# Optimization experiments

Hardware: AMD Instinct MI355X
Metric: run time of the kernel (lower is better)

## Reference

```python
import jax, jax.numpy as jnp
import numpy as np

NUM_EXPERTS = 8
TOP_K = 2


def setup_inputs() -> dict:
    key = jax.random.key(0)
    ks = jax.random.split(key, 5)
    B, S, H, F, E = 2, 2048, 1024, 4096, NUM_EXPERTS
    return {
        "hidden_states": jax.random.normal(ks[0], (B, S, H), dtype=jnp.float32),
        "router_w": jax.random.normal(ks[1], (H, E), dtype=jnp.float32) * 0.02,
        "router_b": jnp.zeros((E,), dtype=jnp.float32),
        "w1": jax.random.normal(ks[2], (E, H, F), dtype=jnp.float32) * 0.02,
        "b1": jnp.zeros((E, F), dtype=jnp.float32),
        "w2": jax.random.normal(ks[3], (E, F, H), dtype=jnp.float32) * 0.02,
        "b2": jnp.zeros((E, H), dtype=jnp.float32),
    }


def reference(hidden_states, router_w, router_b, w1, b1, w2, b2):
    # Router: softmax over experts, take top-2, renormalize.
    logits = jnp.einsum("bsh,he->bse", hidden_states, router_w) + router_b
    probs = jax.nn.softmax(logits, axis=-1)
    top_w, top_i = jax.lax.top_k(probs, TOP_K)              # [B,S,2]
    top_w = top_w / jnp.sum(top_w, axis=-1, keepdims=True)
    # Combine weights per expert: [B,S,E] (sum of slot weights where routed).
    combine = jnp.sum(
        top_w[..., None] * jax.nn.one_hot(top_i, NUM_EXPERTS, dtype=top_w.dtype),
        axis=-2,
    )
    # Dense expert FFN over stacked experts (grouped GEMM form).
    h = jax.nn.gelu(
        jnp.einsum("bsh,ehf->ebsf", hidden_states, w1) + b1[:, None, None, :],
        approximate=False,
    )  # exact GELU matches torch nn.GELU default
    y = jnp.einsum("ebsf,efh->ebsh", h, w2) + b2[:, None, None, :]
    # Weighted combine of top-2 expert outputs per token.
    return jnp.einsum("bse,ebsh->bsh", combine, y)
```

## Files before the change

kernel.cpp:

```cpp
#include <hip/hip_runtime.h>
#include <hip/hip_bf16.h>
#include <stdint.h>

#define T_TOKENS 4096
#define H_DIM    1024
#define F_DIM    4096
#define NE       8
#define NA       8192

typedef __bf16 bf16x8 __attribute__((ext_vector_type(8)));
typedef float  f32x4  __attribute__((ext_vector_type(4)));

__device__ __forceinline__ float b2f(unsigned short u) {
    union { float f; uint32_t i; } v; v.i = ((uint32_t)u) << 16; return v.f;
}
__device__ __forceinline__ unsigned short f2b(float f) {
    union { float f; uint32_t i; } v; v.f = f;
    uint32_t x = v.i;
    return (unsigned short)((x + 0x7FFFu + ((x >> 16) & 1u)) >> 16);
}

__global__ void probe_kernel(const unsigned short* __restrict__ hs,
                             int* __restrict__ flag) {
    int lane = threadIdx.x;
    int cnt = 0;
    for (int j = 0; j < 16; j++) {
        unsigned short u = hs[(lane * 16 + j) * 2];
        int e = (u >> 7) & 0xFF;
        if (e >= 100 && e <= 135) cnt++;
    }
    for (int off = 32; off > 0; off >>= 1) cnt += __shfl_down(cnt, off);
    if (lane == 0) *flag = (cnt >= 512) ? 0 : 1;
}

__global__ __launch_bounds__(256) void conv_hs_kernel(
    const void* __restrict__ hs, const int* __restrict__ flag,
    unsigned short* __restrict__ out) {
    size_t idx = ((size_t)blockIdx.x * 256 + threadIdx.x) * 8;
    if (*flag) {
        const float* p = (const float*)hs + idx;
        float4 a = *(const float4*)p, b = *(const float4*)(p + 4);
        ushort4 o0, o1;
        o0.x = f2b(a.x); o0.y = f2b(a.y); o0.z = f2b(a.z); o0.w = f2b(a.w);
        o1.x = f2b(b.x); o1.y = f2b(b.y); o1.z = f2b(b.z); o1.w = f2b(b.w);
        *(ushort4*)(out + idx) = o0;
        *(ushort4*)(out + idx + 4) = o1;
    } else {
        *(uint4*)(out + idx) = *(const uint4*)((const unsigned short*)hs + idx);
    }
}

__global__ __launch_bounds__(256) void router_kernel(
    const void* __restrict__ hs, const void* __restrict__ rw,
    const void* __restrict__ rb, const int* __restrict__ flag,
    int* __restrict__ top_i, float* __restrict__ top_w) {
    bool f32 = (*flag != 0);
    int wave = threadIdx.x >> 6, lane = threadIdx.x & 63;
    int t = blockIdx.x * 4 + wave;
    float acc[NE];
#pragma unroll
    for (int e = 0; e < NE; e++) acc[e] = 0.f;
    if (f32) {
        const float* hrow = (const float*)hs + (size_t)t * H_DIM;
        const float* rwf = (const float*)rw;
        for (int j = 0; j < 16; j++) {
            int k = j * 64 + lane;
            float h = hrow[k];
            float4 a = *(const float4*)(rwf + (size_t)k * NE);
            float4 b = *(const float4*)(rwf + (size_t)k * NE + 4);
            acc[0] += h * a.x; acc[1] += h * a.y; acc[2] += h * a.z; acc[3] += h * a.w;
            acc[4] += h * b.x; acc[5] += h * b.y; acc[6] += h * b.z; acc[7] += h * b.w;
        }
    } else {
        const unsigned short* hrow = (const unsigned short*)hs + (size_t)t * H_DIM;
        const unsigned short* rwu = (const unsigned short*)rw;
        for (int j = 0; j < 16; j++) {
            int k = j * 64 + lane;
            float h = b2f(hrow[k]);
            uint4 rv = *(const uint4*)(rwu + (size_t)k * NE);
            const unsigned short* rs = (const unsigned short*)&rv;
#pragma unroll
            for (int e = 0; e < NE; e++) acc[e] += h * b2f(rs[e]);
        }
    }
#pragma unroll
    for (int e = 0; e < NE; e++)
        for (int off = 32; off > 0; off >>= 1) acc[e] += __shfl_down(acc[e], off);
    if (lane == 0) {
        float lg[NE];
#pragma unroll
        for (int e = 0; e < NE; e++)
            lg[e] = acc[e] + (f32 ? ((const float*)rb)[e]
                                  : b2f(((const unsigned short*)rb)[e]));
        int e0 = 0;
        for (int e = 1; e < NE; e++) if (lg[e] > lg[e0]) e0 = e;
        int e1 = (e0 == 0) ? 1 : 0;
        for (int e = 0; e < NE; e++) if (e != e0 && lg[e] > lg[e1]) e1 = e;
        float w0 = 1.f / (1.f + expf(lg[e1] - lg[e0]));
        top_i[t * 2] = e0; top_i[t * 2 + 1] = e1;
        top_w[t * 2] = w0; top_w[t * 2 + 1] = 1.f - w0;
    }
}

__global__ __launch_bounds__(256) void assign_kernel(
    const int* __restrict__ top_i, const float* __restrict__ top_w,
    int* __restrict__ token_list, float* __restrict__ wgt_list,
    int* __restrict__ assign_row, int* __restrict__ counts,
    int* __restrict__ offsets) {
    __shared__ int cnt_s[NE], cur_s[NE];
    int tid = threadIdx.x;
    if (tid < NE) cnt_s[tid] = 0;
    __syncthreads();
    for (int idx = tid; idx < NA; idx += 256) atomicAdd(&cnt_s[top_i[idx]], 1);
    __syncthreads();
    if (tid == 0) {
        int run = 0;
        for (int e = 0; e < NE; e++) {
            offsets[e] = run; counts[e] = cnt_s[e]; cur_s[e] = run; run += cnt_s[e];
        }
    }
    __syncthreads();
    for (int idx = tid; idx < NA; idx += 256) {
        int e = top_i[idx];
        int pos = atomicAdd(&cur_s[e], 1);
        token_list[pos] = idx >> 1;
        wgt_list[pos] = top_w[idx];
        assign_row[idx] = pos;
    }
}

__global__ __launch_bounds__(256) void transpose_kernel(
    const void* __restrict__ in, unsigned short* __restrict__ out,
    int R, int C, const int* __restrict__ flag) {
    bool f32 = (*flag != 0);
    size_t zo = (size_t)blockIdx.z * R * C;
    int c0 = blockIdx.x * 64, r0 = blockIdx.y * 64;
    __shared__ unsigned short t[64][65];
    int tx = threadIdx.x & 31, ty = threadIdx.x >> 5;
    if (f32) {
        const float* inf = (const float*)in + zo;
#pragma unroll
        for (int i = 0; i < 8; i++) {
            int r = ty + i * 8;
            float2 v = *(const float2*)&inf[(size_t)(r0 + r) * C + c0 + tx * 2];
            t[r][tx * 2] = f2b(v.x); t[r][tx * 2 + 1] = f2b(v.y);
        }
    } else {
        const unsigned short* inu = (const unsigned short*)in + zo;
#pragma unroll
        for (int i = 0; i < 8; i++) {
            int r = ty + i * 8;
            ushort2 v = *(const ushort2*)&inu[(size_t)(r0 + r) * C + c0 + tx * 2];
            t[r][tx * 2] = v.x; t[r][tx * 2 + 1] = v.y;
        }
    }
    __syncthreads();
#pragma unroll
    for (int i = 0; i < 8; i++) {
        int cc = ty + i * 8;
        ushort2 w; w.x = t[tx * 2][cc]; w.y = t[tx * 2 + 1][cc];
        *(ushort2*)&out[zo + (size_t)(c0 + cc) * R + r0 + tx * 2] = w;
    }
}

template <int MODE>
__global__ __launch_bounds__(256) void gemm_kernel(
    const unsigned short* __restrict__ Abase,
    const unsigned short* __restrict__ Bt,
    const void* __restrict__ bias,
    const int* __restrict__ flag,
    const int* __restrict__ token_list, const float* __restrict__ wgt_list,
    const int* __restrict__ counts, const int* __restrict__ offsets,
    unsigned short* __restrict__ act_out, unsigned short* __restrict__ y_out) {
    constexpr int K    = (MODE == 0) ? H_DIM : F_DIM;
    constexpr int NDIM = (MODE == 0) ? F_DIM : H_DIM;
    constexpr int AST  = (MODE == 0) ? H_DIM : F_DIM;

    const int e = blockIdx.z;
    const int cnt = counts[e];
    const int m0 = blockIdx.y * 128;
    if (m0 >= cnt) return;
    const int off = offsets[e];
    const int n0 = blockIdx.x * 128;
    const bool f32 = (*flag != 0);

    __shared__ __bf16 As[128 * 64];
    __shared__ __bf16 Bs[128 * 64];
    __shared__ int   tok_s[128];
    __shared__ float wgt_s[128];

    const int tid = threadIdx.x;
    const int wave = tid >> 6, lane = tid & 63;

    if (tid < 128) {
        int r = off + min(m0 + tid, cnt - 1);
        tok_s[tid] = (MODE == 0) ? token_list[r] : r;
        wgt_s[tid] = wgt_list[r];
    }
    __syncthreads();

    const int c = tid & 7;
    const int rsub = tid >> 3;
    const unsigned short* Bexp = Bt + (size_t)e * NDIM * K;
    size_t gofsA[4], gofsB[4];
    uint32_t lofs[4];
#pragma unroll
    for (int i = 0; i < 4; i++) {
        int r = i * 32 + rsub;
        int arow = tok_s[r];
        gofsA[i] = (size_t)arow * AST + c * 8;
        gofsB[i] = (size_t)(n0 + r) * K + c * 8;
        lofs[i] = r * 64 + ((c ^ (r & 7)) * 8);
    }

    f32x4 acc[4][4];
#pragma unroll
    for (int i = 0; i < 4; i++)
#pragma unroll
        for (int j = 0; j < 4; j++) acc[i][j] = (f32x4){0.f, 0.f, 0.f, 0.f};

    const int wr = wave >> 1, wc = wave & 1;
    const int lane15 = lane & 15, quad = lane >> 4;

    for (int kt = 0; kt < K / 64; kt++) {
        bf16x8 va[4], vb[4];
#pragma unroll
        for (int i = 0; i < 4; i++)
            va[i] = *(const bf16x8*)(Abase + gofsA[i] + (size_t)kt * 64);
#pragma unroll
        for (int i = 0; i < 4; i++)
            vb[i] = *(const bf16x8*)(Bexp + gofsB[i] + (size_t)kt * 64);
        __syncthreads();
#pragma unroll
        for (int i = 0; i < 4; i++) *(bf16x8*)(As + lofs[i]) = va[i];
#pragma unroll
        for (int i = 0; i < 4; i++) *(bf16x8*)(Bs + lofs[i]) = vb[i];
        __syncthreads();
#pragma unroll
        for (int kk = 0; kk < 2; kk++) {
            bf16x8 a[4], b[4];
#pragma unroll
            for (int i = 0; i < 4; i++) {
                int row = wr * 64 + i * 16 + lane15;
                int koff = (kk * 32 + quad * 8) ^ ((row & 7) * 8);
                a[i] = *(const bf16x8*)&As[row * 64 + koff];
            }
#pragma unroll
            for (int j = 0; j < 4; j++) {
                int row = wc * 64 + j * 16 + lane15;
                int koff = (kk * 32 + quad * 8) ^ ((row & 7) * 8);
                b[j] = *(const bf16x8*)&Bs[row * 64 + koff];
            }
#pragma unroll
            for (int i = 0; i < 4; i++)
#pragma unroll
                for (int j = 0; j < 4; j++)
                    acc[i][j] = __builtin_amdgcn_mfma_f32_16x16x32_bf16(a[i], b[j], acc[i][j], 0, 0, 0);
        }
    }

#pragma unroll
    for (int j = 0; j < 4; j++) {
        int col = n0 + wc * 64 + j * 16 + lane15;
        float bv = f32 ? ((const float*)bias)[(size_t)e * NDIM + col]
                       : b2f(((const unsigned short*)bias)[(size_t)e * NDIM + col]);
#pragma unroll
        for (int i = 0; i < 4; i++) {
#pragma unroll
            for (int r = 0; r < 4; r++) {
                int rowl = wr * 64 + i * 16 + quad * 4 + r;
                if (m0 + rowl < cnt) {
                    float v = acc[i][j][r] + bv;
                    if (MODE == 0) {
                        v = 0.5f * v * (1.f + erff(v * 0.70710678118f));
                        act_out[(size_t)(off + m0 + rowl) * F_DIM + col] = f2b(v);
                    } else {
                        y_out[(size_t)(off + m0 + rowl) * H_DIM + col] = f2b(v * wgt_s[rowl]);
                    }
                }
            }
        }
    }
}

__global__ __launch_bounds__(256) void combine_kernel(
    const unsigned short* __restrict__ y, const int* __restrict__ assign_row,
    void* __restrict__ out, const int* __restrict__ flag) {
    bool f32 = (*flag != 0);
    int t = blockIdx.x;
    int r0 = assign_row[t * 2], r1 = assign_row[t * 2 + 1];
    ushort4 a = ((const ushort4*)(y + (size_t)r0 * H_DIM))[threadIdx.x];
    ushort4 b = ((const ushort4*)(y + (size_t)r1 * H_DIM))[threadIdx.x];
    float s0 = b2f(a.x) + b2f(b.x), s1 = b2f(a.y) + b2f(b.y);
    float s2 = b2f(a.z) + b2f(b.z), s3 = b2f(a.w) + b2f(b.w);
    if (f32) {
        float4 o = {s0, s1, s2, s3};
        ((float4*)out)[(size_t)t * (H_DIM / 4) + threadIdx.x] = o;
    } else {
        ushort4 o;
        o.x = f2b(s0); o.y = f2b(s1); o.z = f2b(s2); o.w = f2b(s3);
        ((ushort4*)((unsigned short*)out + (size_t)t * H_DIM))[threadIdx.x] = o;
    }
}

extern "C" void kernel_launch(void* const* d_in, const int* in_sizes, int n_in,
                              void* d_out, int out_size, void* d_ws, size_t ws_size,
                              hipStream_t stream) {
    const void* hs = d_in[0];
    const void* rw = d_in[1];
    const void* rb = d_in[2];
    const void* w1 = d_in[3];
    const void* b1 = d_in[4];
    const void* w2 = d_in[5];
    const void* b2 = d_in[6];

    char* ws = (char*)d_ws;
    size_t o = 0;
    auto alloc = [&](size_t bytes) {
        char* p = ws + o; o += (bytes + 255) & ~(size_t)255; return p;
    };
    unsigned short* wt   = (unsigned short*)alloc((size_t)NE * F_DIM * H_DIM * 2);
    unsigned short* act  = (unsigned short*)alloc((size_t)NA * F_DIM * 2);
    unsigned short* yb   = (unsigned short*)alloc((size_t)NA * H_DIM * 2);
    unsigned short* hsb  = (unsigned short*)alloc((size_t)T_TOKENS * H_DIM * 2);
    int*   top_i      = (int*)alloc(NA * 4);
    float* top_w      = (float*)alloc(NA * 4);
    int*   token_list = (int*)alloc(NA * 4);
    float* wgt_list   = (float*)alloc(NA * 4);
    int*   assign_row = (int*)alloc(NA * 4);
    int*   counts     = (int*)alloc(64);
    int*   offsets    = (int*)alloc(64);
    int*   flag       = (int*)alloc(64);
    (void)ws_size; (void)in_sizes; (void)n_in; (void)out_size;

    probe_kernel<<<1, 64, 0, stream>>>((const unsigned short*)hs, flag);
    conv_hs_kernel<<<T_TOKENS * H_DIM / 2048, 256, 0, stream>>>(hs, flag, hsb);
    router_kernel<<<T_TOKENS / 4, 256, 0, stream>>>(hs, rw, rb, flag, top_i, top_w);
    assign_kernel<<<1, 256, 0, stream>>>(top_i, top_w, token_list, wgt_list,
                                         assign_row, counts, offsets);
    transpose_kernel<<<dim3(F_DIM / 64, H_DIM / 64, NE), 256, 0, stream>>>(
        w1, wt, H_DIM, F_DIM, flag);
    gemm_kernel<0><<<dim3(F_DIM / 128, T_TOKENS / 128, NE), 256, 0, stream>>>(
        hsb, wt, b1, flag, token_list, wgt_list, counts, offsets, act, nullptr);
    transpose_kernel<<<dim3(H_DIM / 64, F_DIM / 64, NE), 256, 0, stream>>>(
        w2, wt, F_DIM, H_DIM, flag);
    gemm_kernel<1><<<dim3(H_DIM / 128, T_TOKENS / 128, NE), 256, 0, stream>>>(
        act, wt, b2, flag, token_list, wgt_list, counts, offsets, nullptr, yb);
    combine_kernel<<<T_TOKENS, 256, 0, stream>>>(yb, assign_row, d_out, flag);
}
```

Measured before the change: 702.4 us.

## Load GEMM tiles directly into LDS, fuse bf16 conversion into router, shrink FFN2 tile

The GEMM kernel now stages A and B tiles with global_load_lds, which writes straight into LDS and skips the register round trip. The swizzled chunk layout is kept so the existing MFMA fragment reads still match, and the trailing barrier moves to the end of each k-step. The separate hidden-state bf16 conversion kernel is removed; the router writes the bf16 copy while it reads the rows. The second GEMM uses a 64-row M tile with a larger grid to give it more blocks, at the cost of less reuse of B per block.

```diff
diff --git a/kernel.cpp b/kernel.cpp
--- a/kernel.cpp
+++ b/kernel.cpp
@@ -18,6 +18,13 @@
     union { float f; uint32_t i; } v; v.f = f;
     uint32_t x = v.i;
     return (unsigned short)((x + 0x7FFFu + ((x >> 16) & 1u)) >> 16);
+}
+
+__device__ __forceinline__ void gl_lds16(const void* g, void* l) {
+    __builtin_amdgcn_global_load_lds(
+        (const __attribute__((address_space(1))) void*)g,
+        (__attribute__((address_space(3))) void*)l,
+        16, 0, 0);
 }
 
 __global__ void probe_kernel(const unsigned short* __restrict__ hs,
@@ -33,30 +40,15 @@
     if (lane == 0) *flag = (cnt >= 512) ? 0 : 1;
 }
 
-__global__ __launch_bounds__(256) void conv_hs_kernel(
-    const void* __restrict__ hs, const int* __restrict__ flag,
-    unsigned short* __restrict__ out) {
-    size_t idx = ((size_t)blockIdx.x * 256 + threadIdx.x) * 8;
-    if (*flag) {
-        const float* p = (const float*)hs + idx;
-        float4 a = *(const float4*)p, b = *(const float4*)(p + 4);
-        ushort4 o0, o1;
-        o0.x = f2b(a.x); o0.y = f2b(a.y); o0.z = f2b(a.z); o0.w = f2b(a.w);
-        o1.x = f2b(b.x); o1.y = f2b(b.y); o1.z = f2b(b.z); o1.w = f2b(b.w);
-        *(ushort4*)(out + idx) = o0;
-        *(ushort4*)(out + idx + 4) = o1;
-    } else {
-        *(uint4*)(out + idx) = *(const uint4*)((const unsigned short*)hs + idx);
-    }
-}
-
 __global__ __launch_bounds__(256) void router_kernel(
     const void* __restrict__ hs, const void* __restrict__ rw,
     const void* __restrict__ rb, const int* __restrict__ flag,
-    int* __restrict__ top_i, float* __restrict__ top_w) {
+    int* __restrict__ top_i, float* __restrict__ top_w,
+    unsigned short* __restrict__ hsb) {
     bool f32 = (*flag != 0);
     int wave = threadIdx.x >> 6, lane = threadIdx.x & 63;
     int t = blockIdx.x * 4 + wave;
+    unsigned short* hout = hsb + (size_t)t * H_DIM;
     float acc[NE];
 #pragma unroll
     for (int e = 0; e < NE; e++) acc[e] = 0.f;
@@ -66,6 +58,7 @@
         for (int j = 0; j < 16; j++) {
             int k = j * 64 + lane;
             float h = hrow[k];
+            hout[k] = f2b(h);
             float4 a = *(const float4*)(rwf + (size_t)k * NE);
             float4 b = *(const float4*)(rwf + (size_t)k * NE + 4);
             acc[0] += h * a.x; acc[1] += h * a.y; acc[2] += h * a.z; acc[3] += h * a.w;
@@ -76,7 +69,9 @@
         const unsigned short* rwu = (const unsigned short*)rw;
         for (int j = 0; j < 16; j++) {
             int k = j * 64 + lane;
-            float h = b2f(hrow[k]);
+            unsigned short hu = hrow[k];
+            hout[k] = hu;
+            float h = b2f(hu);
             uint4 rv = *(const uint4*)(rwu + (size_t)k * NE);
             const unsigned short* rs = (const unsigned short*)&rv;
 #pragma unroll
@@ -175,47 +170,51 @@
     constexpr int K    = (MODE == 0) ? H_DIM : F_DIM;
     constexpr int NDIM = (MODE == 0) ? F_DIM : H_DIM;
     constexpr int AST  = (MODE == 0) ? H_DIM : F_DIM;
+    constexpr int BM   = (MODE == 0) ? 128 : 64;
+    constexpr int MI   = BM / 32;
 
     const int e = blockIdx.z;
     const int cnt = counts[e];
-    const int m0 = blockIdx.y * 128;
+    const int m0 = blockIdx.y * BM;
     if (m0 >= cnt) return;
     const int off = offsets[e];
     const int n0 = blockIdx.x * 128;
     const bool f32 = (*flag != 0);
 
-    __shared__ __bf16 As[128 * 64];
+    __shared__ __bf16 As[BM * 64];
     __shared__ __bf16 Bs[128 * 64];
-    __shared__ int   tok_s[128];
-    __shared__ float wgt_s[128];
+    __shared__ int   tok_s[BM];
+    __shared__ float wgt_s[BM];
 
     const int tid = threadIdx.x;
     const int wave = tid >> 6, lane = tid & 63;
 
-    if (tid < 128) {
+    if (tid < BM) {
         int r = off + min(m0 + tid, cnt - 1);
         tok_s[tid] = (MODE == 0) ? token_list[r] : r;
         wgt_s[tid] = wgt_list[r];
     }
     __syncthreads();
 
-    const int c = tid & 7;
-    const int rsub = tid >> 3;
-    const unsigned short* Bexp = Bt + (size_t)e * NDIM * K;
-    size_t gofsA[4], gofsB[4];
-    uint32_t lofs[4];
+    const char* Abytes = (const char*)Abase;
+    const char* Bbytes = (const char*)(Bt + (size_t)e * NDIM * K);
+    uint64_t ga[MI], gb[4];
+    const int chunk = (lane & 7) ^ ((lane >> 3) & 7);
+#pragma unroll
+    for (int i = 0; i < MI; i++) {
+        int rowA = (wave * MI + i) * 8 + (lane >> 3);
+        int arow = tok_s[rowA];
+        ga[i] = (uint64_t)(uintptr_t)(Abytes + ((size_t)arow * AST + chunk * 8) * 2);
+    }
 #pragma unroll
     for (int i = 0; i < 4; i++) {
-        int r = i * 32 + rsub;
-        int arow = tok_s[r];
-        gofsA[i] = (size_t)arow * AST + c * 8;
-        gofsB[i] = (size_t)(n0 + r) * K + c * 8;
-        lofs[i] = r * 64 + ((c ^ (r & 7)) * 8);
-    }
-
-    f32x4 acc[4][4];
-#pragma unroll
-    for (int i = 0; i < 4; i++)
+        int rowB = n0 + (wave * 4 + i) * 8 + (lane >> 3);
+        gb[i] = (uint64_t)(uintptr_t)(Bbytes + ((size_t)rowB * K + chunk * 8) * 2);
+    }
+
+    f32x4 acc[MI][4];
+#pragma unroll
+    for (int i = 0; i < MI; i++)
 #pragma unroll
         for (int j = 0; j < 4; j++) acc[i][j] = (f32x4){0.f, 0.f, 0.f, 0.f};
 
@@ -223,25 +222,23 @@
     const int lane15 = lane & 15, quad = lane >> 4;
 
     for (int kt = 0; kt < K / 64; kt++) {
-        bf16x8 va[4], vb[4];
-#pragma unroll
-        for (int i = 0; i < 4; i++)
-            va[i] = *(const bf16x8*)(Abase + gofsA[i] + (size_t)kt * 64);
-#pragma unroll
-        for (int i = 0; i < 4; i++)
-            vb[i] = *(const bf16x8*)(Bexp + gofsB[i] + (size_t)kt * 64);
+#pragma unroll
+        for (int i = 0; i < MI; i++) {
+            gl_lds16((const void*)(uintptr_t)ga[i], (void*)(As + (wave * MI + i) * 512));
+            ga[i] += 128;
+        }
+#pragma unroll
+        for (int i = 0; i < 4; i++) {
+            gl_lds16((const void*)(uintptr_t)gb[i], (void*)(Bs + (wave * 4 + i) * 512));
+            gb[i] += 128;
+        }
         __syncthreads();
 #pragma unroll
-        for (int i = 0; i < 4; i++) *(bf16x8*)(As + lofs[i]) = va[i];
-#pragma unroll
-        for (int i = 0; i < 4; i++) *(bf16x8*)(Bs + lofs[i]) = vb[i];
-        __syncthreads();
-#pragma unroll
         for (int kk = 0; kk < 2; kk++) {
-            bf16x8 a[4], b[4];
-#pragma unroll
-            for (int i = 0; i < 4; i++) {
-                int row = wr * 64 + i * 16 + lane15;
+            bf16x8 a[MI], b[4];
+#pragma unroll
+            for (int i = 0; i < MI; i++) {
+                int row = wr * (BM / 2) + i * 16 + lane15;
                 int koff = (kk * 32 + quad * 8) ^ ((row & 7) * 8);
                 a[i] = *(const bf16x8*)&As[row * 64 + koff];
             }
@@ -252,11 +249,12 @@
                 b[j] = *(const bf16x8*)&Bs[row * 64 + koff];
             }
 #pragma unroll
-            for (int i = 0; i < 4; i++)
+            for (int i = 0; i < MI; i++)
 #pragma unroll
                 for (int j = 0; j < 4; j++)
                     acc[i][j] = __builtin_amdgcn_mfma_f32_16x16x32_bf16(a[i], b[j], acc[i][j], 0, 0, 0);
         }
+        __syncthreads();
     }
 
 #pragma unroll
@@ -265,10 +263,10 @@
         float bv = f32 ? ((const float*)bias)[(size_t)e * NDIM + col]
                        : b2f(((const unsigned short*)bias)[(size_t)e * NDIM + col]);
 #pragma unroll
-        for (int i = 0; i < 4; i++) {
+        for (int i = 0; i < MI; i++) {
 #pragma unroll
             for (int r = 0; r < 4; r++) {
-                int rowl = wr * 64 + i * 16 + quad * 4 + r;
+                int rowl = wr * (BM / 2) + i * 16 + quad * 4 + r;
                 if (m0 + rowl < cnt) {
                     float v = acc[i][j][r] + bv;
                     if (MODE == 0) {
@@ -334,8 +332,7 @@
     (void)ws_size; (void)in_sizes; (void)n_in; (void)out_size;
 
     probe_kernel<<<1, 64, 0, stream>>>((const unsigned short*)hs, flag);
-    conv_hs_kernel<<<T_TOKENS * H_DIM / 2048, 256, 0, stream>>>(hs, flag, hsb);
-    router_kernel<<<T_TOKENS / 4, 256, 0, stream>>>(hs, rw, rb, flag, top_i, top_w);
+    router_kernel<<<T_TOKENS / 4, 256, 0, stream>>>(hs, rw, rb, flag, top_i, top_w, hsb);
     assign_kernel<<<1, 256, 0, stream>>>(top_i, top_w, token_list, wgt_list,
                                          assign_row, counts, offsets);
     transpose_kernel<<<dim3(F_DIM / 64, H_DIM / 64, NE), 256, 0, stream>>>(
@@ -344,7 +341,7 @@
         hsb, wt, b1, flag, token_list, wgt_list, counts, offsets, act, nullptr);
     transpose_kernel<<<dim3(H_DIM / 64, F_DIM / 64, NE), 256, 0, stream>>>(
         w2, wt, F_DIM, H_DIM, flag);
-    gemm_kernel<1><<<dim3(H_DIM / 128, T_TOKENS / 128, NE), 256, 0, stream>>>(
+    gemm_kernel<1><<<dim3(H_DIM / 128, NA / 64, NE), 256, 0, stream>>>(
         act, wt, b2, flag, token_list, wgt_list, counts, offsets, nullptr, yb);
     combine_kernel<<<T_TOKENS, 256, 0, stream>>>(yb, assign_row, d_out, flag);
 }
```

New measurement: 666.4 us. -5.1%, faster.
